# Kernel tuning notes

Hardware: AMD Instinct MI355X
Metric: run time of the kernel (lower is better)

Reference implementation:

```python
import jax, jax.numpy as jnp
import numpy as np

H = 8          # kernel_size == hidden size
NUM_LAYERS = 4
NEG_SLOPE = 0.2


def _gru_scan(x_pre, W_hh, b_hh, reverse):
    """Run a single-direction GRU over time.
    x_pre: (N, T, 3H) precomputed input projections W_ih @ x + b_ih.
    Returns outputs (N, T, H) aligned with input time order.
    PyTorch gate order: [r, z, n].
    """
    N = x_pre.shape[0]

    def step(h, xp):
        gh = h @ W_hh.T + b_hh                      # (N, 3H)
        xr, xz, xn = jnp.split(xp, 3, axis=-1)
        hr, hz, hn = jnp.split(gh, 3, axis=-1)
        r = jax.nn.sigmoid(xr + hr)
        z = jax.nn.sigmoid(xz + hz)
        n = jnp.tanh(xn + r * hn)
        h_new = (1.0 - z) * n + z * h
        return h_new, h_new

    h0 = jnp.zeros((N, H), x_pre.dtype)
    _, ys = jax.lax.scan(step, h0, jnp.swapaxes(x_pre, 0, 1), reverse=reverse)
    return jnp.swapaxes(ys, 0, 1)                   # (N, T, H)


def setup_inputs() -> dict:
    key = jax.random.key(0)
    ks = jax.random.split(key, 16)
    s = 1.0 / np.sqrt(H)  # PyTorch GRU init scale
    u = lambda k, shape: jax.random.uniform(k, shape, jnp.float32, -s, s)
    return {
        "raw": jax.random.normal(ks[0], (32, 400, 4096), jnp.float32),
        "W_ih_l0": u(ks[1], (2, 3 * H, H)),
        "W_hh_l0": u(ks[2], (2, 3 * H, H)),
        "b_ih_l0": u(ks[3], (2, 3 * H)),
        "b_hh_l0": u(ks[4], (2, 3 * H)),
        "W_ih_rest": u(ks[5], (NUM_LAYERS - 1, 2, 3 * H, 2 * H)),
        "W_hh_rest": u(ks[6], (NUM_LAYERS - 1, 2, 3 * H, H)),
        "b_ih_rest": u(ks[7], (NUM_LAYERS - 1, 2, 3 * H)),
        "b_hh_rest": u(ks[8], (NUM_LAYERS - 1, 2, 3 * H)),
        "lin1_w": u(ks[9], (H, 2 * H)),
        "lin1_b": u(ks[10], (H,)),
        "lin2_w": u(ks[11], (H, H)),
        "lin2_b": u(ks[12], (H,)),
    }


def reference(raw, W_ih_l0, W_hh_l0, b_ih_l0, b_hh_l0,
              W_ih_rest, W_hh_rest, b_ih_rest, b_hh_rest,
              lin1_w, lin1_b, lin2_w, lin2_b):
    b, k, L = raw.shape
    T = L // H
    x = raw.reshape(b * k, T, H)                    # (N, T, H)

    for layer in range(NUM_LAYERS):
        if layer == 0:
            Wih, Whh, bih, bhh = W_ih_l0, W_hh_l0, b_ih_l0, b_hh_l0
        else:
            Wih, Whh = W_ih_rest[layer - 1], W_hh_rest[layer - 1]
            bih, bhh = b_ih_rest[layer - 1], b_hh_rest[layer - 1]
        # precompute input projections for the whole sequence (batched GEMM)
        out_f = _gru_scan(x @ Wih[0].T + bih[0], Whh[0], bhh[0], reverse=False)
        out_b = _gru_scan(x @ Wih[1].T + bih[1], Whh[1], bhh[1], reverse=True)
        x = jnp.concatenate([out_f, out_b], axis=-1)  # (N, T, 2H)

    last = x[:, -1, :].reshape(b, k, 2 * H)
    # Dropout is identity in eval mode.
    h = last @ lin1_w.T + lin1_b
    h = jnp.where(h >= 0, h, NEG_SLOPE * h)         # LeakyReLU(0.2)
    return h @ lin2_w.T + lin2_b                    # (b, k, out_size)
```

## Files before the change

kernel.cpp:

```cpp
#include <hip/hip_runtime.h>
#include <type_traits>

#define DEVINL __device__ __forceinline__

typedef __fp16 f16;
typedef __fp16 f16x2 __attribute__((ext_vector_type(2)));
typedef __fp16 f16x8 __attribute__((ext_vector_type(8)));

constexpr int Hh = 8;
constexpr int G3 = 24;
constexpr int TT = 512;

constexpr float SNEG  = -1.44269504088896340736f;
constexpr float SNEG2 = -2.88539008177792681472f;

DEVINL float dot2(f16x2 a, f16x2 b, float c) {
#if __has_builtin(__builtin_amdgcn_fdot2)
    return __builtin_amdgcn_fdot2(a, b, c, false);
#else
    return fmaf((float)a[1], (float)b[1], fmaf((float)a[0], (float)b[0], c));
#endif
}

template <typename InT, int IN_DIM>
DEVINL void load_x(f16x2* d, const InT* p) {
    if constexpr (std::is_same<InT, float>::value) {
        const float4* p4 = (const float4*)p;
#pragma unroll
        for (int q = 0; q < IN_DIM / 4; ++q) {
            float4 v = p4[q];
            d[2 * q]     = __builtin_amdgcn_cvt_pkrtz(v.x, v.y);
            d[2 * q + 1] = __builtin_amdgcn_cvt_pkrtz(v.z, v.w);
        }
    } else {
        const f16x8* p8 = (const f16x8*)p;
#pragma unroll
        for (int c = 0; c < IN_DIM / 8; ++c) {
            f16x8 v = p8[c];
            d[4 * c + 0] = __builtin_shufflevector(v, v, 0, 1);
            d[4 * c + 1] = __builtin_shufflevector(v, v, 2, 3);
            d[4 * c + 2] = __builtin_shufflevector(v, v, 4, 5);
            d[4 * c + 3] = __builtin_shufflevector(v, v, 6, 7);
        }
    }
}

template <typename InT, int IN_DIM, bool LAST>
__global__ __launch_bounds__(64, 2) void gru_scan(
    const InT* __restrict__ x,
    const float* __restrict__ Wih,
    const float* __restrict__ Whh,
    const float* __restrict__ bih,
    const float* __restrict__ bhh,
    f16* __restrict__ out,
    float* __restrict__ last,
    int n)
{
    const int tid   = threadIdx.x;
    const int lane8 = tid & 7;
    const int unit  = blockIdx.x * 8 + (tid >> 3);
    const int dir   = unit >= n ? 1 : 0;
    const int seq   = unit - dir * n;

    const int g0 = lane8, g1 = 8 + lane8, g2 = 16 + lane8;

    __shared__ __align__(16) f16 hsh[64];
    const int hbase = (tid >> 3) * 8;

    const float* Wd = Wih + (size_t)dir * G3 * IN_DIM;
    f16x2 wi0[IN_DIM / 2], wi1[IN_DIM / 2], wi2[IN_DIM / 2];
#pragma unroll
    for (int q = 0; q < IN_DIM / 2; ++q) {
        wi0[q] = __builtin_amdgcn_cvt_pkrtz(Wd[g0 * IN_DIM + 2 * q] * SNEG,
                                            Wd[g0 * IN_DIM + 2 * q + 1] * SNEG);
        wi1[q] = __builtin_amdgcn_cvt_pkrtz(Wd[g1 * IN_DIM + 2 * q] * SNEG,
                                            Wd[g1 * IN_DIM + 2 * q + 1] * SNEG);
        wi2[q] = __builtin_amdgcn_cvt_pkrtz(Wd[g2 * IN_DIM + 2 * q] * SNEG2,
                                            Wd[g2 * IN_DIM + 2 * q + 1] * SNEG2);
    }
    const float* Hd = Whh + (size_t)dir * G3 * Hh;
    f16x2 wh0[Hh / 2], wh1[Hh / 2], wh2[Hh / 2];
#pragma unroll
    for (int q = 0; q < Hh / 2; ++q) {
        wh0[q] = __builtin_amdgcn_cvt_pkrtz(Hd[g0 * Hh + 2 * q] * SNEG,
                                            Hd[g0 * Hh + 2 * q + 1] * SNEG);
        wh1[q] = __builtin_amdgcn_cvt_pkrtz(Hd[g1 * Hh + 2 * q] * SNEG,
                                            Hd[g1 * Hh + 2 * q + 1] * SNEG);
        wh2[q] = __builtin_amdgcn_cvt_pkrtz(Hd[g2 * Hh + 2 * q] * SNEG2,
                                            Hd[g2 * Hh + 2 * q + 1] * SNEG2);
    }
    const float br  = (bih[dir * G3 + g0] + bhh[dir * G3 + g0]) * SNEG;
    const float bz  = (bih[dir * G3 + g1] + bhh[dir * G3 + g1]) * SNEG;
    const float bxn = bih[dir * G3 + g2] * SNEG2;
    const float bhn = bhh[dir * G3 + g2] * SNEG2;

    f16x2 h2[Hh / 2];
#pragma unroll
    for (int q = 0; q < Hh / 2; ++q) h2[q] = f16x2{(f16)0.f, (f16)0.f};
    float hown = 0.f;

    const int t0 = dir ? (TT - 1) : 0;
    const int xstep = dir ? -IN_DIM : IN_DIM;
    const int ostep = dir ? -16 : 16;
    const InT* xp = x + (size_t)(seq * TT + t0) * IN_DIM;
    f16* op = LAST ? nullptr
                   : out + (size_t)(seq * TT + t0) * 16 + dir * 8 + lane8;

    const int steps = (LAST && dir) ? 1 : TT;

    f16x2 xa[IN_DIM / 2], xb[IN_DIM / 2];
    load_x<InT, IN_DIM>(xa, xp); xp += xstep;
    if (steps > 1) { load_x<InT, IN_DIM>(xb, xp); xp += xstep; }

#define GRU_STEP(XV, PF)                                                      \
    {                                                                         \
        float sr = br, sz = bz, xn = bxn;                                     \
        _Pragma("unroll")                                                     \
        for (int q = 0; q < IN_DIM / 2; ++q) {                                \
            sr = dot2(wi0[q], XV[q], sr);                                     \
            sz = dot2(wi1[q], XV[q], sz);                                     \
            xn = dot2(wi2[q], XV[q], xn);                                     \
        }                                                                     \
        if (PF) { load_x<InT, IN_DIM>(XV, xp); xp += xstep; }                 \
        float hn = bhn;                                                       \
        _Pragma("unroll")                                                     \
        for (int q = 0; q < Hh / 2; ++q) {                                    \
            sr = dot2(wh0[q], h2[q], sr);                                     \
            sz = dot2(wh1[q], h2[q], sz);                                     \
            hn = dot2(wh2[q], h2[q], hn);                                     \
        }                                                                     \
        float r  = __builtin_amdgcn_rcpf(1.f + __builtin_amdgcn_exp2f(sr));   \
        float z  = __builtin_amdgcn_rcpf(1.f + __builtin_amdgcn_exp2f(sz));   \
        float vS = fminf(fmaf(r, hn, xn), 60.f);    \
        float e2 = __builtin_amdgcn_exp2f(vS);                                \
        float nn = (1.f - e2) * __builtin_amdgcn_rcpf(1.f + e2);              \
        float hnew = fmaf(z, hown - nn, nn);               \
        hown = hnew;                                                          \
        f16 hf = (f16)hnew;                           \
        if (!LAST) { *op = hf; op += ostep; }                                 \
        hsh[hbase + lane8] = hf;                                              \
        __builtin_amdgcn_wave_barrier();                                      \
        f16x8 hv = *(const f16x8*)&hsh[hbase];                                \
        h2[0] = __builtin_shufflevector(hv, hv, 0, 1);                        \
        h2[1] = __builtin_shufflevector(hv, hv, 2, 3);                        \
        h2[2] = __builtin_shufflevector(hv, hv, 4, 5);                        \
        h2[3] = __builtin_shufflevector(hv, hv, 6, 7);                        \
    }

    int s = 0;
    for (; s + 2 < steps; s += 2) {
        GRU_STEP(xa, true);
        GRU_STEP(xb, true);
    }
    GRU_STEP(xa, false);
    if (steps > 1) GRU_STEP(xb, false);
#undef GRU_STEP

    if (LAST) last[(size_t)seq * 16 + dir * 8 + lane8] = hown;
}

__global__ void head_kernel(const float* __restrict__ last,
                            const float* __restrict__ w1, const float* __restrict__ b1,
                            const float* __restrict__ w2, const float* __restrict__ b2,
                            float* __restrict__ out, int n)
{
    int i = blockIdx.x * blockDim.x + threadIdx.x;
    if (i >= n) return;
    const float* v = last + (size_t)i * 16;
    float h1[8];
#pragma unroll
    for (int j = 0; j < 8; ++j) {
        float a = b1[j];
#pragma unroll
        for (int k = 0; k < 16; ++k) a = fmaf(w1[j * 16 + k], v[k], a);
        h1[j] = a >= 0.f ? a : 0.2f * a;
    }
#pragma unroll
    for (int j = 0; j < 8; ++j) {
        float o = b2[j];
#pragma unroll
        for (int k = 0; k < 8; ++k) o = fmaf(w2[j * 8 + k], h1[k], o);
        out[(size_t)i * 8 + j] = o;
    }
}

extern "C" void kernel_launch(void* const* d_in, const int* in_sizes, int n_in,
                              void* d_out, int out_size, void* d_ws, size_t ws_size,
                              hipStream_t stream)
{
    const float* raw  = (const float*)d_in[0];
    const float* Wih0 = (const float*)d_in[1];
    const float* Whh0 = (const float*)d_in[2];
    const float* bih0 = (const float*)d_in[3];
    const float* bhh0 = (const float*)d_in[4];
    const float* WihR = (const float*)d_in[5];
    const float* WhhR = (const float*)d_in[6];
    const float* bihR = (const float*)d_in[7];
    const float* bhhR = (const float*)d_in[8];
    const float* w1   = (const float*)d_in[9];
    const float* b1   = (const float*)d_in[10];
    const float* w2   = (const float*)d_in[11];
    const float* b2   = (const float*)d_in[12];

    const int n = in_sizes[0] / (TT * Hh);
    const size_t bufE = (size_t)n * TT * 16;
    dim3 blk(64);
    dim3 grid((unsigned)((2 * n) / 8));
    dim3 hblk(256);
    dim3 hgrid((unsigned)((n + 255) / 256));

    f16* bufA   = (f16*)d_ws;
    f16* bufB   = bufA + bufE;
    float* lastb = (float*)(bufB + bufE);

    gru_scan<float, 8, false><<<grid, blk, 0, stream>>>(
        raw, Wih0, Whh0, bih0, bhh0, bufA, (float*)nullptr, n);
    gru_scan<f16, 16, false><<<grid, blk, 0, stream>>>(
        bufA, WihR + 0 * 2 * G3 * 16, WhhR + 0 * 2 * G3 * 8,
        bihR + 0 * 2 * G3, bhhR + 0 * 2 * G3, bufB, (float*)nullptr, n);
    gru_scan<f16, 16, false><<<grid, blk, 0, stream>>>(
        bufB, WihR + 1 * 2 * G3 * 16, WhhR + 1 * 2 * G3 * 8,
        bihR + 1 * 2 * G3, bhhR + 1 * 2 * G3, bufA, (float*)nullptr, n);
    gru_scan<f16, 16, true><<<grid, blk, 0, stream>>>(
        bufA, WihR + 2 * 2 * G3 * 16, WhhR + 2 * 2 * G3 * 8,
        bihR + 2 * 2 * G3, bhhR + 2 * 2 * G3, (f16*)nullptr, lastb, n);
    head_kernel<<<hgrid, hblk, 0, stream>>>(
        lastb, w1, b1, w2, b2, (float*)d_out, n);
}
```

Baseline: 1.419 ms.

## Split GRU gate dot products across lane pairs with swizzle reduction

Each sequence-direction unit now uses 16 lanes instead of 8. Each lane pair splits the input and hidden dot products in half and combines the partial sums with a ds_swizzle xor-8 exchange. This shortens the serial per-step arithmetic chain in the recurrence and doubles the number of waves, which should hide latency better; launch bounds are raised to match. The cost is duplicated activation math, an extra cross-lane exchange on every timestep, and twice as many blocks.

```diff
diff --git a/kernel.cpp b/kernel.cpp
--- a/kernel.cpp
+++ b/kernel.cpp
@@ -5,6 +5,7 @@
 
 typedef __fp16 f16;
 typedef __fp16 f16x2 __attribute__((ext_vector_type(2)));
+typedef __fp16 f16x4 __attribute__((ext_vector_type(4)));
 typedef __fp16 f16x8 __attribute__((ext_vector_type(8)));
 
 constexpr int Hh = 8;
@@ -22,31 +23,27 @@
 #endif
 }
 
+DEVINL float swz8(float v) {
+    return __int_as_float(__builtin_amdgcn_ds_swizzle(__float_as_int(v), 0x201F));
+}
+
 template <typename InT, int IN_DIM>
-DEVINL void load_x(f16x2* d, const InT* p) {
+DEVINL void load_xh(f16x2* d, const InT* p) {
     if constexpr (std::is_same<InT, float>::value) {
-        const float4* p4 = (const float4*)p;
-#pragma unroll
-        for (int q = 0; q < IN_DIM / 4; ++q) {
-            float4 v = p4[q];
-            d[2 * q]     = __builtin_amdgcn_cvt_pkrtz(v.x, v.y);
-            d[2 * q + 1] = __builtin_amdgcn_cvt_pkrtz(v.z, v.w);
-        }
+        float4 v = *(const float4*)p;
+        d[0] = __builtin_amdgcn_cvt_pkrtz(v.x, v.y);
+        d[1] = __builtin_amdgcn_cvt_pkrtz(v.z, v.w);
     } else {
-        const f16x8* p8 = (const f16x8*)p;
-#pragma unroll
-        for (int c = 0; c < IN_DIM / 8; ++c) {
-            f16x8 v = p8[c];
-            d[4 * c + 0] = __builtin_shufflevector(v, v, 0, 1);
-            d[4 * c + 1] = __builtin_shufflevector(v, v, 2, 3);
-            d[4 * c + 2] = __builtin_shufflevector(v, v, 4, 5);
-            d[4 * c + 3] = __builtin_shufflevector(v, v, 6, 7);
-        }
+        f16x8 v = *(const f16x8*)p;
+        d[0] = __builtin_shufflevector(v, v, 0, 1);
+        d[1] = __builtin_shufflevector(v, v, 2, 3);
+        d[2] = __builtin_shufflevector(v, v, 4, 5);
+        d[3] = __builtin_shufflevector(v, v, 6, 7);
     }
 }
 
 template <typename InT, int IN_DIM, bool LAST>
-__global__ __launch_bounds__(64, 2) void gru_scan(
+__global__ __launch_bounds__(64, 6) void gru_scan(
     const InT* __restrict__ x,
     const float* __restrict__ Wih,
     const float* __restrict__ Whh,
@@ -56,95 +53,104 @@
     float* __restrict__ last,
     int n)
 {
-    const int tid   = threadIdx.x;
-    const int lane8 = tid & 7;
-    const int unit  = blockIdx.x * 8 + (tid >> 3);
-    const int dir   = unit >= n ? 1 : 0;
-    const int seq   = unit - dir * n;
-
-    const int g0 = lane8, g1 = 8 + lane8, g2 = 16 + lane8;
-
-    __shared__ __align__(16) f16 hsh[64];
-    const int hbase = (tid >> 3) * 8;
+    constexpr int HALF = IN_DIM / 2;
+    constexpr int QP   = HALF / 2;
+
+    const int tid  = threadIdx.x;
+    const int u    = tid >> 4;
+    const int l16  = tid & 15;
+    const int p    = l16 & 7;
+    const int hi   = l16 >> 3;
+    const int unit = blockIdx.x * 4 + u;
+    const int dir  = unit >= n ? 1 : 0;
+    const int seq  = unit - dir * n;
+
+    const int g0 = p, g1 = 8 + p, g2 = 16 + p;
+
+    __shared__ __align__(8) f16 hsh[64];
 
     const float* Wd = Wih + (size_t)dir * G3 * IN_DIM;
-    f16x2 wi0[IN_DIM / 2], wi1[IN_DIM / 2], wi2[IN_DIM / 2];
-#pragma unroll
-    for (int q = 0; q < IN_DIM / 2; ++q) {
-        wi0[q] = __builtin_amdgcn_cvt_pkrtz(Wd[g0 * IN_DIM + 2 * q] * SNEG,
-                                            Wd[g0 * IN_DIM + 2 * q + 1] * SNEG);
-        wi1[q] = __builtin_amdgcn_cvt_pkrtz(Wd[g1 * IN_DIM + 2 * q] * SNEG,
-                                            Wd[g1 * IN_DIM + 2 * q + 1] * SNEG);
-        wi2[q] = __builtin_amdgcn_cvt_pkrtz(Wd[g2 * IN_DIM + 2 * q] * SNEG2,
-                                            Wd[g2 * IN_DIM + 2 * q + 1] * SNEG2);
+    const int k0 = hi * HALF;
+    f16x2 wi0[QP], wi1[QP], wi2[QP];
+#pragma unroll
+    for (int q = 0; q < QP; ++q) {
+        const int k = k0 + 2 * q;
+        wi0[q] = __builtin_amdgcn_cvt_pkrtz(Wd[g0 * IN_DIM + k] * SNEG,
+                                            Wd[g0 * IN_DIM + k + 1] * SNEG);
+        wi1[q] = __builtin_amdgcn_cvt_pkrtz(Wd[g1 * IN_DIM + k] * SNEG,
+                                            Wd[g1 * IN_DIM + k + 1] * SNEG);
+        wi2[q] = __builtin_amdgcn_cvt_pkrtz(Wd[g2 * IN_DIM + k] * SNEG2,
+                                            Wd[g2 * IN_DIM + k + 1] * SNEG2);
     }
     const float* Hd = Whh + (size_t)dir * G3 * Hh;
-    f16x2 wh0[Hh / 2], wh1[Hh / 2], wh2[Hh / 2];
-#pragma unroll
-    for (int q = 0; q < Hh / 2; ++q) {
-        wh0[q] = __builtin_amdgcn_cvt_pkrtz(Hd[g0 * Hh + 2 * q] * SNEG,
-                                            Hd[g0 * Hh + 2 * q + 1] * SNEG);
-        wh1[q] = __builtin_amdgcn_cvt_pkrtz(Hd[g1 * Hh + 2 * q] * SNEG,
-                                            Hd[g1 * Hh + 2 * q + 1] * SNEG);
-        wh2[q] = __builtin_amdgcn_cvt_pkrtz(Hd[g2 * Hh + 2 * q] * SNEG2,
-                                            Hd[g2 * Hh + 2 * q + 1] * SNEG2);
-    }
-    const float br  = (bih[dir * G3 + g0] + bhh[dir * G3 + g0]) * SNEG;
-    const float bz  = (bih[dir * G3 + g1] + bhh[dir * G3 + g1]) * SNEG;
-    const float bxn = bih[dir * G3 + g2] * SNEG2;
-    const float bhn = bhh[dir * G3 + g2] * SNEG2;
-
-    f16x2 h2[Hh / 2];
-#pragma unroll
-    for (int q = 0; q < Hh / 2; ++q) h2[q] = f16x2{(f16)0.f, (f16)0.f};
+    const int j0 = hi * 4;
+    f16x2 wh0[2], wh1[2], wh2[2];
+#pragma unroll
+    for (int q = 0; q < 2; ++q) {
+        const int j = j0 + 2 * q;
+        wh0[q] = __builtin_amdgcn_cvt_pkrtz(Hd[g0 * Hh + j] * SNEG,
+                                            Hd[g0 * Hh + j + 1] * SNEG);
+        wh1[q] = __builtin_amdgcn_cvt_pkrtz(Hd[g1 * Hh + j] * SNEG,
+                                            Hd[g1 * Hh + j + 1] * SNEG);
+        wh2[q] = __builtin_amdgcn_cvt_pkrtz(Hd[g2 * Hh + j] * SNEG2,
+                                            Hd[g2 * Hh + j + 1] * SNEG2);
+    }
+    const float br  = hi ? 0.f : (bih[dir * G3 + g0] + bhh[dir * G3 + g0]) * SNEG;
+    const float bz  = hi ? 0.f : (bih[dir * G3 + g1] + bhh[dir * G3 + g1]) * SNEG;
+    const float bxn = hi ? 0.f : bih[dir * G3 + g2] * SNEG2;
+    const float bhn = hi ? 0.f : bhh[dir * G3 + g2] * SNEG2;
+
+    f16x2 h2[2];
+    h2[0] = f16x2{(f16)0.f, (f16)0.f};
+    h2[1] = f16x2{(f16)0.f, (f16)0.f};
     float hown = 0.f;
 
     const int t0 = dir ? (TT - 1) : 0;
     const int xstep = dir ? -IN_DIM : IN_DIM;
     const int ostep = dir ? -16 : 16;
-    const InT* xp = x + (size_t)(seq * TT + t0) * IN_DIM;
+    const InT* xp = x + (size_t)(seq * TT + t0) * IN_DIM + k0;
     f16* op = LAST ? nullptr
-                   : out + (size_t)(seq * TT + t0) * 16 + dir * 8 + lane8;
+                   : out + (size_t)(seq * TT + t0) * 16 + dir * 8 + p;
 
     const int steps = (LAST && dir) ? 1 : TT;
 
-    f16x2 xa[IN_DIM / 2], xb[IN_DIM / 2];
-    load_x<InT, IN_DIM>(xa, xp); xp += xstep;
-    if (steps > 1) { load_x<InT, IN_DIM>(xb, xp); xp += xstep; }
+    f16x2 xa[QP], xb[QP];
+    load_xh<InT, IN_DIM>(xa, xp); xp += xstep;
+    if (steps > 1) { load_xh<InT, IN_DIM>(xb, xp); xp += xstep; }
 
 #define GRU_STEP(XV, PF)                                                      \
     {                                                                         \
         float sr = br, sz = bz, xn = bxn;                                     \
         _Pragma("unroll")                                                     \
-        for (int q = 0; q < IN_DIM / 2; ++q) {                                \
+        for (int q = 0; q < QP; ++q) {                                        \
             sr = dot2(wi0[q], XV[q], sr);                                     \
             sz = dot2(wi1[q], XV[q], sz);                                     \
             xn = dot2(wi2[q], XV[q], xn);                                     \
         }                                                                     \
-        if (PF) { load_x<InT, IN_DIM>(XV, xp); xp += xstep; }                 \
+        if (PF) { load_xh<InT, IN_DIM>(XV, xp); xp += xstep; }                \
         float hn = bhn;                                                       \
         _Pragma("unroll")                                                     \
-        for (int q = 0; q < Hh / 2; ++q) {                                    \
+        for (int q = 0; q < 2; ++q) {                                         \
             sr = dot2(wh0[q], h2[q], sr);                                     \
             sz = dot2(wh1[q], h2[q], sz);                                     \
             hn = dot2(wh2[q], h2[q], hn);                                     \
         }                                                                     \
+        sr += swz8(sr); sz += swz8(sz);                                       \
+        xn += swz8(xn); hn += swz8(hn);                                       \
         float r  = __builtin_amdgcn_rcpf(1.f + __builtin_amdgcn_exp2f(sr));   \
         float z  = __builtin_amdgcn_rcpf(1.f + __builtin_amdgcn_exp2f(sz));   \
-        float vS = fminf(fmaf(r, hn, xn), 60.f);    \
+        float vS = fminf(fmaf(r, hn, xn), 60.f);               \
         float e2 = __builtin_amdgcn_exp2f(vS);                                \
         float nn = (1.f - e2) * __builtin_amdgcn_rcpf(1.f + e2);              \
         float hnew = fmaf(z, hown - nn, nn);               \
         hown = hnew;                                                          \
-        f16 hf = (f16)hnew;                           \
-        if (!LAST) { *op = hf; op += ostep; }                                 \
-        hsh[hbase + lane8] = hf;                                              \
+        f16 hf = (f16)hnew;                                                   \
+        if (!LAST) { if (!hi) *op = hf; op += ostep; }                        \
+        hsh[u * 16 + hi * 8 + p] = hf;                                        \
         __builtin_amdgcn_wave_barrier();                                      \
-        f16x8 hv = *(const f16x8*)&hsh[hbase];                                \
+        f16x4 hv = *(const f16x4*)&hsh[u * 16 + hi * 4];                      \
         h2[0] = __builtin_shufflevector(hv, hv, 0, 1);                        \
         h2[1] = __builtin_shufflevector(hv, hv, 2, 3);                        \
-        h2[2] = __builtin_shufflevector(hv, hv, 4, 5);                        \
-        h2[3] = __builtin_shufflevector(hv, hv, 6, 7);                        \
     }
 
     int s = 0;
@@ -156,7 +162,7 @@
     if (steps > 1) GRU_STEP(xb, false);
 #undef GRU_STEP
 
-    if (LAST) last[(size_t)seq * 16 + dir * 8 + lane8] = hown;
+    if (LAST && !hi) last[(size_t)seq * 16 + dir * 8 + p] = hown;
 }
 
 __global__ void head_kernel(const float* __restrict__ last,
@@ -205,7 +211,7 @@
     const int n = in_sizes[0] / (TT * Hh);
     const size_t bufE = (size_t)n * TT * 16;
     dim3 blk(64);
-    dim3 grid((unsigned)((2 * n) / 8));
+    dim3 grid((unsigned)((2 * n) / 4));
     dim3 hblk(256);
     dim3 hgrid((unsigned)((n + 255) / 256));
 
```

Result: slower. 1.629 ms (+14.8%).

## Split hidden-state buffers per direction and use 128-thread blocks

Applied to the files above, without the earlier changes.

Intermediate layer outputs are stored in separate forward and backward buffers with an 8-halves row stride, instead of one interleaved buffer with a 16-halves stride. Each direction's per-step 16-byte store is now contiguous across time, and the next layer loads its input as two 16-byte reads from the two buffers. Blocks grow from 64 to 128 threads (16 sequences per block) and the launch bounds change to (128,4), which alters occupancy and register limits. The aim is denser global write and read patterns per step, at the cost of two input streams per step.

```diff
diff --git a/kernel.cpp b/kernel.cpp
--- a/kernel.cpp
+++ b/kernel.cpp
@@ -22,55 +22,63 @@
 #endif
 }
 
-template <typename InT, int IN_DIM>
-DEVINL void load_x(f16x2* d, const InT* p) {
+template <typename InT, bool TWO_IN>
+DEVINL void load_x(f16x2* d, const InT* pf, const InT* pb) {
     if constexpr (std::is_same<InT, float>::value) {
-        const float4* p4 = (const float4*)p;
-#pragma unroll
-        for (int q = 0; q < IN_DIM / 4; ++q) {
-            float4 v = p4[q];
-            d[2 * q]     = __builtin_amdgcn_cvt_pkrtz(v.x, v.y);
-            d[2 * q + 1] = __builtin_amdgcn_cvt_pkrtz(v.z, v.w);
+        const float4* p4 = (const float4*)pf;
+        float4 v0 = p4[0], v1 = p4[1];
+        d[0] = __builtin_amdgcn_cvt_pkrtz(v0.x, v0.y);
+        d[1] = __builtin_amdgcn_cvt_pkrtz(v0.z, v0.w);
+        d[2] = __builtin_amdgcn_cvt_pkrtz(v1.x, v1.y);
+        d[3] = __builtin_amdgcn_cvt_pkrtz(v1.z, v1.w);
+    } else {
+        f16x8 a = *(const f16x8*)pf;
+        d[0] = __builtin_shufflevector(a, a, 0, 1);
+        d[1] = __builtin_shufflevector(a, a, 2, 3);
+        d[2] = __builtin_shufflevector(a, a, 4, 5);
+        d[3] = __builtin_shufflevector(a, a, 6, 7);
+        if constexpr (TWO_IN) {
+            f16x8 b = *(const f16x8*)pb;
+            d[4] = __builtin_shufflevector(b, b, 0, 1);
+            d[5] = __builtin_shufflevector(b, b, 2, 3);
+            d[6] = __builtin_shufflevector(b, b, 4, 5);
+            d[7] = __builtin_shufflevector(b, b, 6, 7);
         }
-    } else {
-        const f16x8* p8 = (const f16x8*)p;
-#pragma unroll
-        for (int c = 0; c < IN_DIM / 8; ++c) {
-            f16x8 v = p8[c];
-            d[4 * c + 0] = __builtin_shufflevector(v, v, 0, 1);
-            d[4 * c + 1] = __builtin_shufflevector(v, v, 2, 3);
-            d[4 * c + 2] = __builtin_shufflevector(v, v, 4, 5);
-            d[4 * c + 3] = __builtin_shufflevector(v, v, 6, 7);
-        }
-    }
-}
-
-template <typename InT, int IN_DIM, bool LAST>
-__global__ __launch_bounds__(64, 2) void gru_scan(
-    const InT* __restrict__ x,
+    }
+}
+
+template <typename InT, bool TWO_IN, bool LAST>
+__global__ __launch_bounds__(128, 4) void gru_scan(
+    const InT* __restrict__ xf,
+    const InT* __restrict__ xb,
     const float* __restrict__ Wih,
     const float* __restrict__ Whh,
     const float* __restrict__ bih,
     const float* __restrict__ bhh,
-    f16* __restrict__ out,
+    f16* __restrict__ outF,
+    f16* __restrict__ outB,
     float* __restrict__ last,
     int n)
 {
+    constexpr int IN_DIM = TWO_IN ? 16 : 8;
+    constexpr int QW = IN_DIM / 2;
+
     const int tid   = threadIdx.x;
     const int lane8 = tid & 7;
-    const int unit  = blockIdx.x * 8 + (tid >> 3);
+    const int grp   = tid >> 3;
+    const int unit  = blockIdx.x * 16 + grp;
     const int dir   = unit >= n ? 1 : 0;
     const int seq   = unit - dir * n;
 
     const int g0 = lane8, g1 = 8 + lane8, g2 = 16 + lane8;
 
-    __shared__ __align__(16) f16 hsh[64];
-    const int hbase = (tid >> 3) * 8;
+    __shared__ __align__(16) f16 hsh[128];
+    const int hbase = grp * 8;
 
     const float* Wd = Wih + (size_t)dir * G3 * IN_DIM;
-    f16x2 wi0[IN_DIM / 2], wi1[IN_DIM / 2], wi2[IN_DIM / 2];
-#pragma unroll
-    for (int q = 0; q < IN_DIM / 2; ++q) {
+    f16x2 wi0[QW], wi1[QW], wi2[QW];
+#pragma unroll
+    for (int q = 0; q < QW; ++q) {
         wi0[q] = __builtin_amdgcn_cvt_pkrtz(Wd[g0 * IN_DIM + 2 * q] * SNEG,
                                             Wd[g0 * IN_DIM + 2 * q + 1] * SNEG);
         wi1[q] = __builtin_amdgcn_cvt_pkrtz(Wd[g1 * IN_DIM + 2 * q] * SNEG,
@@ -100,28 +108,37 @@
     float hown = 0.f;
 
     const int t0 = dir ? (TT - 1) : 0;
-    const int xstep = dir ? -IN_DIM : IN_DIM;
-    const int ostep = dir ? -16 : 16;
-    const InT* xp = x + (size_t)(seq * TT + t0) * IN_DIM;
+    const int xstep = dir ? -8 : 8;
+    const int ostep = dir ? -8 : 8;
+    const InT* xpf = xf + (size_t)(seq * TT + t0) * 8;
+    const InT* xpb = TWO_IN ? (xb + (size_t)(seq * TT + t0) * 8)
+                            : (const InT*)nullptr;
     f16* op = LAST ? nullptr
-                   : out + (size_t)(seq * TT + t0) * 16 + dir * 8 + lane8;
+                   : (dir ? outB : outF) + (size_t)(seq * TT + t0) * 8 + lane8;
 
     const int steps = (LAST && dir) ? 1 : TT;
 
-    f16x2 xa[IN_DIM / 2], xb[IN_DIM / 2];
-    load_x<InT, IN_DIM>(xa, xp); xp += xstep;
-    if (steps > 1) { load_x<InT, IN_DIM>(xb, xp); xp += xstep; }
+    f16x2 xA[QW], xB[QW];
+    load_x<InT, TWO_IN>(xA, xpf, xpb);
+    xpf += xstep; if constexpr (TWO_IN) xpb += xstep;
+    if (steps > 1) {
+        load_x<InT, TWO_IN>(xB, xpf, xpb);
+        xpf += xstep; if constexpr (TWO_IN) xpb += xstep;
+    }
 
 #define GRU_STEP(XV, PF)                                                      \
     {                                                                         \
         float sr = br, sz = bz, xn = bxn;                                     \
         _Pragma("unroll")                                                     \
-        for (int q = 0; q < IN_DIM / 2; ++q) {                                \
+        for (int q = 0; q < QW; ++q) {                                        \
             sr = dot2(wi0[q], XV[q], sr);                                     \
             sz = dot2(wi1[q], XV[q], sz);                                     \
             xn = dot2(wi2[q], XV[q], xn);                                     \
         }                                                                     \
-        if (PF) { load_x<InT, IN_DIM>(XV, xp); xp += xstep; }                 \
+        if (PF) {                                                             \
+            load_x<InT, TWO_IN>(XV, xpf, xpb);                                \
+            xpf += xstep; if constexpr (TWO_IN) xpb += xstep;                 \
+        }                                                                     \
         float hn = bhn;                                                       \
         _Pragma("unroll")                                                     \
         for (int q = 0; q < Hh / 2; ++q) {                                    \
@@ -131,7 +148,7 @@
         }                                                                     \
         float r  = __builtin_amdgcn_rcpf(1.f + __builtin_amdgcn_exp2f(sr));   \
         float z  = __builtin_amdgcn_rcpf(1.f + __builtin_amdgcn_exp2f(sz));   \
-        float vS = fminf(fmaf(r, hn, xn), 60.f);    \
+        float vS = fminf(fmaf(r, hn, xn), 60.f);               \
         float e2 = __builtin_amdgcn_exp2f(vS);                                \
         float nn = (1.f - e2) * __builtin_amdgcn_rcpf(1.f + e2);              \
         float hnew = fmaf(z, hown - nn, nn);               \
@@ -149,11 +166,11 @@
 
     int s = 0;
     for (; s + 2 < steps; s += 2) {
-        GRU_STEP(xa, true);
-        GRU_STEP(xb, true);
-    }
-    GRU_STEP(xa, false);
-    if (steps > 1) GRU_STEP(xb, false);
+        GRU_STEP(xA, true);
+        GRU_STEP(xB, true);
+    }
+    GRU_STEP(xA, false);
+    if (steps > 1) GRU_STEP(xB, false);
 #undef GRU_STEP
 
     if (LAST) last[(size_t)seq * 16 + dir * 8 + lane8] = hown;
@@ -203,27 +220,31 @@
     const float* b2   = (const float*)d_in[12];
 
     const int n = in_sizes[0] / (TT * Hh);
-    const size_t bufE = (size_t)n * TT * 16;
-    dim3 blk(64);
-    dim3 grid((unsigned)((2 * n) / 8));
+    const size_t hbE = (size_t)n * TT * 8;
+    dim3 blk(128);
+    dim3 grid((unsigned)((2 * n) / 16));
     dim3 hblk(256);
     dim3 hgrid((unsigned)((n + 255) / 256));
 
-    f16* bufA   = (f16*)d_ws;
-    f16* bufB   = bufA + bufE;
-    float* lastb = (float*)(bufB + bufE);
-
-    gru_scan<float, 8, false><<<grid, blk, 0, stream>>>(
-        raw, Wih0, Whh0, bih0, bhh0, bufA, (float*)nullptr, n);
-    gru_scan<f16, 16, false><<<grid, blk, 0, stream>>>(
-        bufA, WihR + 0 * 2 * G3 * 16, WhhR + 0 * 2 * G3 * 8,
-        bihR + 0 * 2 * G3, bhhR + 0 * 2 * G3, bufB, (float*)nullptr, n);
-    gru_scan<f16, 16, false><<<grid, blk, 0, stream>>>(
-        bufB, WihR + 1 * 2 * G3 * 16, WhhR + 1 * 2 * G3 * 8,
-        bihR + 1 * 2 * G3, bhhR + 1 * 2 * G3, bufA, (float*)nullptr, n);
-    gru_scan<f16, 16, true><<<grid, blk, 0, stream>>>(
-        bufA, WihR + 2 * 2 * G3 * 16, WhhR + 2 * 2 * G3 * 8,
-        bihR + 2 * 2 * G3, bhhR + 2 * 2 * G3, (f16*)nullptr, lastb, n);
+    f16* AF = (f16*)d_ws;
+    f16* AB = AF + hbE;
+    f16* BF = AB + hbE;
+    f16* BB = BF + hbE;
+    float* lastb = (float*)(BB + hbE);
+
+    gru_scan<float, false, false><<<grid, blk, 0, stream>>>(
+        raw, (const float*)nullptr, Wih0, Whh0, bih0, bhh0,
+        AF, AB, (float*)nullptr, n);
+    gru_scan<f16, true, false><<<grid, blk, 0, stream>>>(
+        AF, AB, WihR + 0 * 2 * G3 * 16, WhhR + 0 * 2 * G3 * 8,
+        bihR + 0 * 2 * G3, bhhR + 0 * 2 * G3, BF, BB, (float*)nullptr, n);
+    gru_scan<f16, true, false><<<grid, blk, 0, stream>>>(
+        BF, BB, WihR + 1 * 2 * G3 * 16, WhhR + 1 * 2 * G3 * 8,
+        bihR + 1 * 2 * G3, bhhR + 1 * 2 * G3, AF, AB, (float*)nullptr, n);
+    gru_scan<f16, true, true><<<grid, blk, 0, stream>>>(
+        AF, AB, WihR + 2 * 2 * G3 * 16, WhhR + 2 * 2 * G3 * 8,
+        bihR + 2 * 2 * G3, bhhR + 2 * 2 * G3,
+        (f16*)nullptr, (f16*)nullptr, lastb, n);
     head_kernel<<<hgrid, hblk, 0, stream>>>(
         lastb, w1, b1, w2, b2, (float*)d_out, n);
 }
```

New measurement: 1.375 ms. 1.03x faster.
